# Kernel tuning notes

Measured on AMD Instinct MI355X. Metric: run time of the kernel, lower is better.

The kernel has to match this reference:

```python
import jax, jax.numpy as jnp
import numpy as np

B, E, C, R_REL = 2, 1024, 128, 32

def setup_inputs() -> dict:
    key = jax.random.key(0)
    kx, kr = jax.random.split(key)
    x = jax.random.normal(kx, (B, E, C), dtype=jnp.float32)
    R = jax.random.normal(kr, (R_REL, E, E), dtype=jnp.float32)
    return {"x": x, "R": R}

def reference(x, R):
    # Gram matrix over the feature axis: G[b,s,o] = sum_c x[b,s,c] x[b,o,c]
    G = jnp.einsum('bsc,boc->bso', x, x)  # (B, E, E)
    # Broadcast-scale by relation tensor: out[b,s,r,o] = G[b,s,o] * R[r,s,o]
    scores = G[:, :, None, :] * R[None, :, :, :].transpose(0, 2, 1, 3)  # (B, E, R, E)
    return scores
```

## Files before the change

kernel.cpp:

```cpp
#include <hip/hip_runtime.h>

#define B_SZ 2
#define E_SZ 1024
#define C_SZ 128
#define R_REL 32
#define TS 64
#define TO 64

__global__ __launch_bounds__(256, 2) void rescal_fused(
        const float* __restrict__ x,
        const float* __restrict__ R,
        float* __restrict__ out) {
    __shared__ float xs[TS][C_SZ + 4];
    __shared__ float xo[TO][C_SZ + 4];

    const int b  = blockIdx.z;
    const int s0 = blockIdx.y * TS;
    const int o0 = blockIdx.x * TO;
    const int tid = threadIdx.x;

    const float4* src_s = (const float4*)(x + (size_t)b * E_SZ * C_SZ + (size_t)s0 * C_SZ);
    const float4* src_o = (const float4*)(x + (size_t)b * E_SZ * C_SZ + (size_t)o0 * C_SZ);
    #pragma unroll
    for (int i = tid; i < TS * (C_SZ / 4); i += 256) {
        const int row = i >> 5;
        const int col = (i & 31) << 2;
        *(float4*)&xs[row][col] = src_s[i];
        *(float4*)&xo[row][col] = src_o[i];
    }
    __syncthreads();

    const int tx = tid & 15;
    const int ty = tid >> 4;
    const int si = ty << 2;
    const int oj = tx << 2;

    float acc[4][4];
    #pragma unroll
    for (int ii = 0; ii < 4; ++ii)
        #pragma unroll
        for (int jj = 0; jj < 4; ++jj) acc[ii][jj] = 0.f;

    #pragma unroll 4
    for (int c = 0; c < C_SZ; c += 4) {
        float4 a[4], bb[4];
        #pragma unroll
        for (int ii = 0; ii < 4; ++ii) a[ii]  = *(const float4*)&xs[si + ii][c];
        #pragma unroll
        for (int jj = 0; jj < 4; ++jj) bb[jj] = *(const float4*)&xo[oj + jj][c];
        #pragma unroll
        for (int ii = 0; ii < 4; ++ii) {
            #pragma unroll
            for (int jj = 0; jj < 4; ++jj) {
                acc[ii][jj] += a[ii].x * bb[jj].x + a[ii].y * bb[jj].y
                             + a[ii].z * bb[jj].z + a[ii].w * bb[jj].w;
            }
        }
    }

    const size_t out_base = ((size_t)b * E_SZ + (size_t)s0) * (size_t)(R_REL * E_SZ) + o0;
    #pragma unroll 1
    for (int r = 0; r < R_REL; ++r) {
        const float* Rp = R + (size_t)r * (E_SZ * E_SZ) + (size_t)s0 * E_SZ + o0;
        float* op = out + out_base + (size_t)r * E_SZ;
        #pragma unroll
        for (int ii = 0; ii < 4; ++ii) {
            const float4 rv = *(const float4*)(Rp + (size_t)(si + ii) * E_SZ + oj);
            float4 ov;
            ov.x = acc[ii][0] * rv.x;
            ov.y = acc[ii][1] * rv.y;
            ov.z = acc[ii][2] * rv.z;
            ov.w = acc[ii][3] * rv.w;
            *(float4*)(op + (size_t)(si + ii) * (R_REL * E_SZ) + oj) = ov;
        }
    }
}

extern "C" void kernel_launch(void* const* d_in, const int* in_sizes, int n_in,
                              void* d_out, int out_size, void* d_ws, size_t ws_size,
                              hipStream_t stream) {
    const float* x = (const float*)d_in[0];
    const float* R = (const float*)d_in[1];
    float* out = (float*)d_out;
    dim3 grid(E_SZ / TO, E_SZ / TS, B_SZ);
    rescal_fused<<<grid, 256, 0, stream>>>(x, R, out);
}
```

Baseline: 387.8 us.

## Split fused Gram-scale kernel into Gram kernel plus streaming scale kernel

The fused kernel is split into two. One kernel computes the Gram matrix G into workspace. A second, fully coalesced elementwise kernel streams R once and writes the output for both batches, so each R element is read once instead of once per batch. This targets the strided, low-occupancy store pattern and the duplicated R reads of the fused epilogue, at the cost of a G round-trip through memory and an extra launch.

```diff
diff --git a/kernel.cpp b/kernel.cpp
--- a/kernel.cpp
+++ b/kernel.cpp
@@ -7,10 +7,9 @@
 #define TS 64
 #define TO 64
 
-__global__ __launch_bounds__(256, 2) void rescal_fused(
+__global__ __launch_bounds__(256, 2) void compute_g(
         const float* __restrict__ x,
-        const float* __restrict__ R,
-        float* __restrict__ out) {
+        float* __restrict__ G) {
     __shared__ float xs[TS][C_SZ + 4];
     __shared__ float xo[TO][C_SZ + 4];
 
@@ -49,31 +48,41 @@
         #pragma unroll
         for (int jj = 0; jj < 4; ++jj) bb[jj] = *(const float4*)&xo[oj + jj][c];
         #pragma unroll
-        for (int ii = 0; ii < 4; ++ii) {
+        for (int ii = 0; ii < 4; ++ii)
             #pragma unroll
-            for (int jj = 0; jj < 4; ++jj) {
+            for (int jj = 0; jj < 4; ++jj)
                 acc[ii][jj] += a[ii].x * bb[jj].x + a[ii].y * bb[jj].y
                              + a[ii].z * bb[jj].z + a[ii].w * bb[jj].w;
-            }
-        }
     }
 
-    const size_t out_base = ((size_t)b * E_SZ + (size_t)s0) * (size_t)(R_REL * E_SZ) + o0;
-    #pragma unroll 1
-    for (int r = 0; r < R_REL; ++r) {
-        const float* Rp = R + (size_t)r * (E_SZ * E_SZ) + (size_t)s0 * E_SZ + o0;
-        float* op = out + out_base + (size_t)r * E_SZ;
-        #pragma unroll
-        for (int ii = 0; ii < 4; ++ii) {
-            const float4 rv = *(const float4*)(Rp + (size_t)(si + ii) * E_SZ + oj);
-            float4 ov;
-            ov.x = acc[ii][0] * rv.x;
-            ov.y = acc[ii][1] * rv.y;
-            ov.z = acc[ii][2] * rv.z;
-            ov.w = acc[ii][3] * rv.w;
-            *(float4*)(op + (size_t)(si + ii) * (R_REL * E_SZ) + oj) = ov;
-        }
+    float* gp = G + ((size_t)b * E_SZ + (size_t)(s0 + si)) * E_SZ + o0 + oj;
+    #pragma unroll
+    for (int ii = 0; ii < 4; ++ii) {
+        float4 gv;
+        gv.x = acc[ii][0]; gv.y = acc[ii][1]; gv.z = acc[ii][2]; gv.w = acc[ii][3];
+        *(float4*)(gp + (size_t)ii * E_SZ) = gv;
     }
+}
+
+__global__ __launch_bounds__(256, 8) void scale_stream(
+        const float4* __restrict__ G4,
+        const float4* __restrict__ R4,
+        float4* __restrict__ out4) {
+    const int idx = blockIdx.x * 256 + threadIdx.x;
+    const int o4 = idx & 255;
+    const int r  = (idx >> 8) & 31;
+    const int s  = idx >> 13;
+
+    const float4 rv = R4[((size_t)r << 18) + ((size_t)s << 8) + o4];
+    const float4 g0 = G4[((size_t)s << 8) + o4];
+    const float4 g1 = G4[262144 + ((size_t)s << 8) + o4];
+
+    float4 v0, v1;
+    v0.x = g0.x * rv.x; v0.y = g0.y * rv.y; v0.z = g0.z * rv.z; v0.w = g0.w * rv.w;
+    v1.x = g1.x * rv.x; v1.y = g1.y * rv.y; v1.z = g1.z * rv.z; v1.w = g1.w * rv.w;
+
+    out4[idx]           = v0;
+    out4[idx + 8388608] = v1;
 }
 
 extern "C" void kernel_launch(void* const* d_in, const int* in_sizes, int n_in,
@@ -82,6 +91,12 @@
     const float* x = (const float*)d_in[0];
     const float* R = (const float*)d_in[1];
     float* out = (float*)d_out;
-    dim3 grid(E_SZ / TO, E_SZ / TS, B_SZ);
-    rescal_fused<<<grid, 256, 0, stream>>>(x, R, out);
+    float* G = (float*)d_ws;
+
+    dim3 gridA(E_SZ / TO, E_SZ / TS, B_SZ);
+    compute_g<<<gridA, 256, 0, stream>>>(x, G);
+
+    const int total4 = E_SZ * R_REL * (E_SZ / 4);
+    scale_stream<<<total4 / 256, 256, 0, stream>>>(
+        (const float4*)G, (const float4*)R, (float4*)out);
 }
```

Measured after the change: 388.7 us. About the same (+0.2%).
